# Kernel tuning notes

Hardware: AMD Instinct MI355X
Metric: run time of the kernel (lower is better)

The kernel has to match this reference:

```python
import jax, jax.numpy as jnp
import numpy as np

COST_CLASS, COST_BBOX, COST_MASK = 1.0, 5.0, 2.0
EPS = 1e-6


def setup_inputs() -> dict:
    key = jax.random.key(0)
    k = jax.random.split(key, 8)
    B, Q, M, C1, H, W = 8, 300, 100, 81, 128, 128
    pred_logits = jax.random.normal(k[0], (B, Q, C1), jnp.float32)
    # boxes as valid xyxy in [0,1]: lo in [0,.5], size in [0,.5]
    plo = jax.random.uniform(k[1], (B, Q, 2)) * 0.5
    psz = jax.random.uniform(k[2], (B, Q, 2)) * 0.5
    pred_boxes = jnp.concatenate([plo, plo + psz], axis=-1)
    pred_masks = jax.random.normal(k[3], (B, Q, H, W), jnp.float32)
    gt_labels = jax.random.randint(k[4], (B, M), 0, C1, dtype=jnp.int32)
    glo = jax.random.uniform(k[5], (B, M, 2)) * 0.5
    gsz = jax.random.uniform(k[6], (B, M, 2)) * 0.5
    gt_boxes = jnp.concatenate([glo, glo + gsz], axis=-1)
    gt_masks = (jax.random.uniform(k[7], (B, M, H, W)) > 0.5).astype(jnp.float32)
    valid = jnp.ones((B, M), jnp.bool_)
    return dict(pred_logits=pred_logits, pred_boxes=pred_boxes, pred_masks=pred_masks,
                gt_labels=gt_labels, gt_boxes=gt_boxes, gt_masks=gt_masks, valid=valid)


def _giou(b1, b2):
    # b1 [Q,4], b2 [M,4] (xyxy) -> [Q,M] generalized IoU
    lt = jnp.maximum(b1[:, None, :2], b2[None, :, :2])
    rb = jnp.minimum(b1[:, None, 2:], b2[None, :, 2:])
    wh = jnp.clip(rb - lt, 0.0)
    inter = wh[..., 0] * wh[..., 1]
    a1 = (b1[:, 2] - b1[:, 0]) * (b1[:, 3] - b1[:, 1])
    a2 = (b2[:, 2] - b2[:, 0]) * (b2[:, 3] - b2[:, 1])
    union = a1[:, None] + a2[None, :] - inter
    iou = inter / (union + EPS)
    ltm = jnp.minimum(b1[:, None, :2], b2[None, :, :2])
    rbm = jnp.maximum(b1[:, None, 2:], b2[None, :, 2:])
    whm = jnp.clip(rbm - ltm, 0.0)
    am = whm[..., 0] * whm[..., 1]
    return iou - (am - union) / (am + EPS)


@jax.jit
def _cost_matrix(pred_logits, pred_boxes, pred_masks, gt_labels, gt_boxes, gt_masks):
    B, Q = pred_logits.shape[:2]
    M = gt_labels.shape[1]
    probs = jax.nn.softmax(pred_logits, axis=-1)                      # [B,Q,C+1]
    idx = jnp.broadcast_to(gt_labels[:, None, :].astype(jnp.int32), (B, Q, M))
    cost_class = -jnp.take_along_axis(probs, idx, axis=2)             # [B,Q,M]
    # L1 cdist
    cost_bbox = jnp.abs(pred_boxes[:, :, None, :] - gt_boxes[:, None, :, :]).sum(-1)
    cost_giou = -jax.vmap(_giou)(pred_boxes, gt_boxes)                # [B,Q,M]
    # dice cost
    pm = jax.nn.sigmoid(pred_masks).reshape(B, Q, -1)                 # [B,Q,HW]
    gm = gt_masks.reshape(B, M, -1).astype(pm.dtype)                  # [B,M,HW]
    num = 2.0 * jnp.einsum('bqc,bmc->bqm', pm, gm)
    den = pm.sum(-1)[:, :, None] + gm.sum(-1)[:, None, :]
    cost_mask = 1.0 - num / (den + EPS)
    # NOTE: faithful to source quirk -- giou term is folded into cost_bbox
    # and therefore weighted by COST_BBOX.
    return (COST_CLASS * cost_class + COST_BBOX * (cost_bbox + cost_giou)
            + COST_MASK * cost_mask)


def _hungarian(cost):
    # Jonker-Volgenant style shortest-augmenting-path assignment (e-maxx).
    # cost: np [n,m] with n <= m. Returns p[m]: row assigned to each col (-1 if none).
    n, m = cost.shape
    u = np.zeros(n)
    v = np.zeros(m)
    p = np.full(m, -1, np.int64)
    for i in range(n):
        minv = np.full(m, np.inf)
        way = np.full(m, -1, np.int64)
        used = np.zeros(m, bool)
        cur_row, j0 = i, -1
        while True:
            cur = cost[cur_row] - u[cur_row] - v
            upd = (~used) & (cur < minv)
            minv[upd] = cur[upd]
            way[upd] = j0
            mv = np.where(used, np.inf, minv)
            j1 = int(np.argmin(mv))
            delta = mv[j1]
            u[i] += delta
            uj = np.nonzero(used)[0]
            if uj.size:
                u[p[uj]] += delta
                v[uj] -= delta
            minv[~used] -= delta
            used[j1] = True
            j0 = j1
            cur_row = p[j1]
            if cur_row == -1:
                break
        j = j0
        while j != -1:
            jp = way[j]
            p[j] = p[jp] if jp != -1 else i
            j = jp
    return p


def reference(pred_logits, pred_boxes, pred_masks, gt_labels, gt_boxes, gt_masks, valid):
    # valid is all-ones (num_gt == max_objects for every sample), so the
    # per-sample variable-size slicing in the torch loop reduces to full M.
    C = _cost_matrix(pred_logits, pred_boxes, pred_masks, gt_labels, gt_boxes, gt_masks)
    Cn = np.asarray(C, dtype=np.float64)
    preds, gts = [], []
    for b in range(Cn.shape[0]):
        # solve on transpose: rows = gt (M=100) <= cols = queries (Q=300)
        p = _hungarian(Cn[b].T)            # p[q] = matched gt index or -1
        q = np.nonzero(p >= 0)[0]          # sorted pred indices (scipy convention)
        preds.append(q)
        gts.append(p[q])
    pred_idx = jnp.asarray(np.stack(preds), dtype=jnp.int32)  # [B, M]
    gt_idx = jnp.asarray(np.stack(gts), dtype=jnp.int32)      # [B, M]
    return C, pred_idx, gt_idx
```

## Files before the change

### kernel.cpp

```cpp
#include <hip/hip_runtime.h>

#define HW 16384
#define NQ 300
#define NM 100
#define NB 8
#define NC 81
#define KCH 1024
#define NKC 16
#define CTP 304

typedef __attribute__((ext_vector_type(8))) short frag8;
typedef __attribute__((ext_vector_type(4))) float float4v;
typedef __attribute__((ext_vector_type(4))) unsigned short ushort4v;

__device__ __forceinline__ unsigned short f2bf(float f) {
  union { float f; unsigned u; } c; c.f = f;
  unsigned r = c.u + 0x7FFFu + ((c.u >> 16) & 1u);
  return (unsigned short)(r >> 16);
}

__global__ __launch_bounds__(256) void gmprep_kernel(
    const float* __restrict__ gmask, unsigned short* __restrict__ gm,
    float* __restrict__ gsum) {
  int row = blockIdx.x;
  int t = threadIdx.x;
  const float4v* src = (const float4v*)(gmask + (size_t)row * HW);
  unsigned short* dst = gm + (size_t)row * HW;
  float s = 0.f;
  for (int i = t; i < HW / 4; i += 256) {
    float4v x = src[i];
    s += (x.x + x.y) + (x.z + x.w);
    ushort4v o = { f2bf(x.x), f2bf(x.y), f2bf(x.z), f2bf(x.w) };
    *(ushort4v*)(dst + i * 4) = o;
  }
  for (int off = 32; off > 0; off >>= 1) s += __shfl_xor(s, off, 64);
  __shared__ float red[4];
  int wave = t >> 6, lane = t & 63;
  if (lane == 0) red[wave] = s;
  __syncthreads();
  if (t == 0) gsum[row] = (red[0] + red[1]) + (red[2] + red[3]);
}

__global__ __launch_bounds__(256) void softmax_kernel(
    const float* __restrict__ logits, float* __restrict__ probs) {
  int wave = threadIdx.x >> 6, lane = threadIdx.x & 63;
  int row = blockIdx.x * 4 + wave;
  const float* in = logits + (size_t)row * NC;
  float x0 = (lane < NC) ? in[lane] : -1e30f;
  float x1 = (lane + 64 < NC) ? in[lane + 64] : -1e30f;
  float mx = fmaxf(x0, x1);
  for (int off = 32; off > 0; off >>= 1) mx = fmaxf(mx, __shfl_xor(mx, off, 64));
  float e0 = (lane < NC) ? __expf(x0 - mx) : 0.f;
  float e1 = (lane + 64 < NC) ? __expf(x1 - mx) : 0.f;
  float s = e0 + e1;
  for (int off = 32; off > 0; off >>= 1) s += __shfl_xor(s, off, 64);
  float inv = 1.f / s;
  if (lane < NC) probs[(size_t)row * NC + lane] = e0 * inv;
  if (lane + 64 < NC) probs[(size_t)row * NC + lane + 64] = e1 * inv;
}

__global__ __launch_bounds__(64) void dot_kernel(
    const float* __restrict__ pmask, const unsigned short* __restrict__ gm,
    float* __restrict__ dotv, float* __restrict__ psum) {
  int qt = blockIdx.x;
  int b = blockIdx.y >> 4, kc = blockIdx.y & 15;
  int lane = threadIdx.x;
  int q0 = qt * 16;
  int row_a = q0 + (lane & 15);
  int ra = (row_a < NQ) ? row_a : NQ - 1;
  int koff = (lane >> 4) * 8;
  const float* pA = pmask + ((size_t)b * NQ + ra) * HW + kc * KCH + koff;
  const unsigned short* pB0 = gm + (size_t)b * NM * HW + kc * KCH + koff;
  const unsigned short* pB[7];
#pragma unroll
  for (int mt = 0; mt < 7; ++mt) {
    int row_b = mt * 16 + (lane & 15);
    int rb = (row_b < NM) ? row_b : NM - 1;
    pB[mt] = pB0 + (size_t)rb * HW;
  }
  float4v acc[7];
#pragma unroll
  for (int mt = 0; mt < 7; ++mt) acc[mt] = (float4v){0.f, 0.f, 0.f, 0.f};
  float asum = 0.f;
#pragma unroll 2
  for (int k = 0; k < KCH; k += 32) {
    float4v x0 = *(const float4v*)(pA + k);
    float4v x1 = *(const float4v*)(pA + k + 4);
    float s0 = 1.f / (1.f + __expf(-x0.x));
    float s1 = 1.f / (1.f + __expf(-x0.y));
    float s2 = 1.f / (1.f + __expf(-x0.z));
    float s3 = 1.f / (1.f + __expf(-x0.w));
    float s4 = 1.f / (1.f + __expf(-x1.x));
    float s5 = 1.f / (1.f + __expf(-x1.y));
    float s6 = 1.f / (1.f + __expf(-x1.z));
    float s7 = 1.f / (1.f + __expf(-x1.w));
    asum += ((s0 + s1) + (s2 + s3)) + ((s4 + s5) + (s6 + s7));
    frag8 a;
    a[0] = (short)f2bf(s0); a[1] = (short)f2bf(s1);
    a[2] = (short)f2bf(s2); a[3] = (short)f2bf(s3);
    a[4] = (short)f2bf(s4); a[5] = (short)f2bf(s5);
    a[6] = (short)f2bf(s6); a[7] = (short)f2bf(s7);
#pragma unroll
    for (int mt = 0; mt < 7; ++mt) {
      frag8 bb = *(const frag8*)(pB[mt] + k);
      acc[mt] = __builtin_amdgcn_mfma_f32_16x16x32_bf16(a, bb, acc[mt], 0, 0, 0);
    }
  }
  if (row_a < NQ) unsafeAtomicAdd(&psum[b * NQ + row_a], asum);
#pragma unroll
  for (int mt = 0; mt < 7; ++mt) {
    int cm = mt * 16 + (lane & 15);
    if (cm < NM) {
#pragma unroll
      for (int r = 0; r < 4; ++r) {
        int cq = q0 + (lane >> 4) * 4 + r;
        if (cq < NQ)
          unsafeAtomicAdd(&dotv[((size_t)b * NQ + cq) * NM + cm], acc[mt][r]);
      }
    }
  }
}

__global__ __launch_bounds__(256) void combine_kernel(
    const float* __restrict__ dotv, const float* __restrict__ psum,
    const float* __restrict__ gsum, const float* __restrict__ probs,
    const int* __restrict__ labels, const float* __restrict__ pboxes,
    const float* __restrict__ gboxes, float* __restrict__ outC,
    float* __restrict__ ct) {
  int idx = blockIdx.x * 256 + threadIdx.x;
  if (idx >= NB * NQ * NM) return;
  int b = idx / (NQ * NM);
  int r = idx - b * (NQ * NM);
  int q = r / NM;
  int m = r - q * NM;
  float num = 2.f * dotv[idx];
  float den = psum[b * NQ + q] + gsum[b * NM + m];
  float cmask = 1.f - num / (den + 1e-6f);
  int lab = labels[b * NM + m];
  float cclass = -probs[((size_t)b * NQ + q) * NC + lab];
  const float* pb = pboxes + ((size_t)b * NQ + q) * 4;
  const float* gb = gboxes + ((size_t)b * NM + m) * 4;
  float p0 = pb[0], p1 = pb[1], p2 = pb[2], p3 = pb[3];
  float g0 = gb[0], g1 = gb[1], g2 = gb[2], g3 = gb[3];
  float cbbox = fabsf(p0 - g0) + fabsf(p1 - g1) + fabsf(p2 - g2) + fabsf(p3 - g3);
  float iw = fmaxf(fminf(p2, g2) - fmaxf(p0, g0), 0.f);
  float ih = fmaxf(fminf(p3, g3) - fmaxf(p1, g1), 0.f);
  float inter = iw * ih;
  float a1 = (p2 - p0) * (p3 - p1), a2 = (g2 - g0) * (g3 - g1);
  float uni = a1 + a2 - inter;
  float iou = inter / (uni + 1e-6f);
  float aw = fmaxf(fmaxf(p2, g2) - fminf(p0, g0), 0.f);
  float ah = fmaxf(fmaxf(p3, g3) - fminf(p1, g1), 0.f);
  float am = aw * ah;
  float giou = iou - (am - uni) / (am + 1e-6f);
  float C = cclass + 5.f * (cbbox - giou) + 2.f * cmask;
  outC[idx] = C;
  ct[((size_t)b * NM + m) * CTP + q] = C;
}

__device__ __forceinline__ float wave_fmin_bcast(float x) {
  int t;
  t = __builtin_amdgcn_update_dpp(__float_as_int(x), __float_as_int(x), 0x111, 0xf, 0xf, false);
  x = fminf(x, __int_as_float(t));
  t = __builtin_amdgcn_update_dpp(__float_as_int(x), __float_as_int(x), 0x112, 0xf, 0xf, false);
  x = fminf(x, __int_as_float(t));
  t = __builtin_amdgcn_update_dpp(__float_as_int(x), __float_as_int(x), 0x114, 0xf, 0xf, false);
  x = fminf(x, __int_as_float(t));
  t = __builtin_amdgcn_update_dpp(__float_as_int(x), __float_as_int(x), 0x118, 0xf, 0xf, false);
  x = fminf(x, __int_as_float(t));
  t = __builtin_amdgcn_update_dpp(__float_as_int(x), __float_as_int(x), 0x142, 0xf, 0xf, false);
  x = fminf(x, __int_as_float(t));
  t = __builtin_amdgcn_update_dpp(__float_as_int(x), __float_as_int(x), 0x143, 0xf, 0xf, false);
  x = fminf(x, __int_as_float(t));
  return __int_as_float(__builtin_amdgcn_readlane(__float_as_int(x), 63));
}

extern __shared__ char hsmem[];
__global__ __launch_bounds__(64) void hungarian_kernel(
    const float* __restrict__ ct, float* __restrict__ out) {
  float* cost   = (float*)hsmem;
  float* u      = (float*)(hsmem + 121600);
  int*   p      = (int*)(hsmem + 122000);
  int*   way    = (int*)(hsmem + 123280);
  int*   colOwn = (int*)(hsmem + 124560);
  int*   queue  = (int*)(hsmem + 125840);
  int*   qmisc  = (int*)(hsmem + 127440);
  int*   flist  = colOwn;
  const int b = blockIdx.x;
  const int lane = threadIdx.x;
  const float INF = __builtin_inff();

  {
    const float4v* a4 = (const float4v*)(ct + (size_t)b * NM * CTP);
    float4v* c4 = (float4v*)cost;
    for (int i = lane; i < NM * CTP / 4; i += 64) c4[i] = a4[i];
  }
#pragma unroll
  for (int w = 0; w < 5; ++w) {
    p[lane + 64 * w] = -1;
    colOwn[lane + 64 * w] = 0x7fffffff;
  }
  if (lane == 0) { qmisc[0] = 0; qmisc[1] = 0; }
  float v[5];
#pragma unroll
  for (int w = 0; w < 5; ++w) v[w] = 0.f;
  __syncthreads();

  int rarg0 = 0, rarg1 = 0;
  {
    int i = lane;
    float mv = INF; int cj = 0;
    for (int j = 0; j < NQ; ++j) {
      float c = cost[i * CTP + j];
      if (c < mv) { mv = c; cj = j; }
    }
    u[i] = mv; rarg0 = cj;
  }
  if (lane < NM - 64) {
    int i = lane + 64;
    float mv = INF; int cj = 0;
    for (int j = 0; j < NQ; ++j) {
      float c = cost[i * CTP + j];
      if (c < mv) { mv = c; cj = j; }
    }
    u[i] = mv; rarg1 = cj;
  }
  atomicMin(&colOwn[rarg0], lane);
  if (lane < NM - 64) atomicMin(&colOwn[rarg1], lane + 64);
  __syncthreads();
  int free0 = 0, free1 = 0;
  {
    bool won = (colOwn[rarg0] == lane);
    if (won) p[rarg0] = lane;
    if (lane < NM) {}
    free0 = won ? 0 : 1;
  }
  int rowUsed0 = free0 ? 0 : 1;
  int rowUsed1 = 0;
  if (lane < NM - 64) {
    bool won = (colOwn[rarg1] == lane + 64);
    if (won) p[rarg1] = lane + 64;
    rowUsed1 = won ? 1 : 0;
    free1 = won ? 0 : 1;
  }
  __shared__ int rowUsedA[NM];
  rowUsedA[lane < NM ? lane : 0] = 0;
  rowUsedA[lane] = rowUsed0;
  if (lane < NM - 64) rowUsedA[lane + 64] = rowUsed1;
  {
    unsigned long long m0 = __ballot(free0 != 0);
    if (free0) queue[__popcll(m0 & ((1ull << lane) - 1ull))] = lane;
    int base = (int)__popcll(m0);
    unsigned long long m1 = __ballot(free1 != 0);
    if (free1) queue[base + (int)__popcll(m1 & ((1ull << lane) - 1ull))] = lane + 64;
    base += (int)__popcll(m1);
    if (lane == 0) qmisc[1] = base;
  }

  int pops = 0;
  while (true) {
    __syncthreads();
    int h = qmisc[0], t = qmisc[1];
    if (h >= t || pops >= 192) break;
    int i = queue[h];
    ++pops;
    if (lane == 0) qmisc[0] = h + 1;
    float tv[5];
    float m1 = INF, m2 = INF;
#pragma unroll
    for (int w = 0; w < 5; ++w) {
      int j = lane + 64 * w;
      float tt = (j < NQ) ? (cost[i * CTP + j] - v[w]) : INF;
      tv[w] = tt;
      if (tt < m1) { m2 = m1; m1 = tt; } else if (tt < m2) m2 = tt;
    }
    float m1g = wave_fmin_bcast(m1);
    int j1 = -1;
#pragma unroll
    for (int w = 0; w < 5; ++w) {
      unsigned long long mk = __ballot(tv[w] == m1g);
      if (j1 < 0 && mk) j1 = (int)__builtin_ctzll(mk) + 64 * w;
    }
    float c2c = INF;
#pragma unroll
    for (int w = 0; w < 5; ++w)
      if (lane + 64 * w != j1) c2c = fminf(c2c, tv[w]);
    float c2 = wave_fmin_bcast(c2c);
    float delta = (c2 > m1g) ? (c2 - m1g) : 0.f;
    int i1 = p[j1];
    if (i1 >= 0 && delta <= 0.f) {
      if (lane == 0) u[i] = c2;
      continue;
    }
#pragma unroll
    for (int w = 0; w < 5; ++w) if (lane + 64 * w == j1) v[w] -= delta;
    if (lane == 0) {
      u[i] = c2;
      p[j1] = i;
      rowUsedA[i] = 1;
      if (i1 >= 0) { rowUsedA[i1] = 0; queue[t] = i1; qmisc[1] = t + 1; }
    }
  }
  __syncthreads();

  int nfree;
  {
    int r0 = rowUsedA[lane];
    int r1 = (lane < NM - 64) ? rowUsedA[lane + 64] : 1;
    unsigned long long m0 = __ballot(r0 == 0);
    if (!r0) flist[__popcll(m0 & ((1ull << lane) - 1ull))] = lane;
    int base = (int)__popcll(m0);
    unsigned long long m1 = __ballot(r1 == 0);
    if (!r1) flist[base + (int)__popcll(m1 & ((1ull << lane) - 1ull))] = lane + 64;
    nfree = base + (int)__popcll(m1);
  }
  __syncthreads();

  int pr0, pr1, pr2, pr3, pr4;
  float ur0, ur1;
  pr0 = p[lane]; pr1 = p[lane + 64]; pr2 = p[lane + 128];
  pr3 = p[lane + 192]; pr4 = p[lane + 256];
  ur0 = u[lane];
  ur1 = (lane < NM - 64) ? u[lane + 64] : 0.f;

  for (int fi = 0; fi < nfree; ++fi) {
    int i = flist[fi];
    float dv[5]; int usedR[5];
#pragma unroll
    for (int w = 0; w < 5; ++w) {
      int j = lane + 64 * w;
      dv[w] = INF;
      usedR[w] = (j >= NQ) ? 1 : 0;
      way[j] = -1;
    }
    float S = 0.f;
    int nr = i, j0 = -1;
    while (true) {
      float urow;
      {
        int bits = (nr < 64)
            ? __builtin_amdgcn_readlane(__float_as_int(ur0), nr & 63)
            : __builtin_amdgcn_readlane(__float_as_int(ur1), nr & 63);
        urow = __int_as_float(bits);
      }
      int base = nr * CTP;
      float c0 = cost[base + lane];
      float c1 = cost[base + lane + 64];
      float c2_ = cost[base + lane + 128];
      float c3 = cost[base + lane + 192];
      float c4 = cost[base + lane + 256];
      float cr[5] = {c0, c1, c2_, c3, c4};
      float cmin = INF;
#pragma unroll
      for (int w = 0; w < 5; ++w) {
        if (!usedR[w]) {
          float cand = S + cr[w] - urow - v[w];
          if (cand < dv[w]) { dv[w] = cand; way[lane + 64 * w] = j0; }
          cmin = fminf(cmin, dv[w]);
        }
      }
      float m = wave_fmin_bcast(cmin);
      int j1 = -1;
#pragma unroll
      for (int w = 0; w < 5; ++w) {
        unsigned long long mk = __ballot(!usedR[w] && dv[w] == m);
        if (j1 < 0 && mk) j1 = (int)__builtin_ctzll(mk) + 64 * w;
      }
      S = m;
#pragma unroll
      for (int w = 0; w < 5; ++w) if (lane + 64 * w == j1) usedR[w] = 1;
      j0 = j1;
      int nr2;
      {
        int sl = j1 >> 6, ln = j1 & 63;
        if (sl == 0)      nr2 = __builtin_amdgcn_readlane(pr0, ln);
        else if (sl == 1) nr2 = __builtin_amdgcn_readlane(pr1, ln);
        else if (sl == 2) nr2 = __builtin_amdgcn_readlane(pr2, ln);
        else if (sl == 3) nr2 = __builtin_amdgcn_readlane(pr3, ln);
        else              nr2 = __builtin_amdgcn_readlane(pr4, ln);
      }
      if (nr2 < 0) break;
      nr = nr2;
    }
#pragma unroll
    for (int w = 0; w < 5; ++w) {
      int j = lane + 64 * w;
      if (j < NQ && usedR[w]) {
        float amt = S - dv[w];
        v[w] -= amt;
        int pj = (w == 0) ? pr0 : (w == 1) ? pr1 : (w == 2) ? pr2
               : (w == 3) ? pr3 : pr4;
        if (pj >= 0) u[pj] += amt;
      }
    }
    if (lane == 0) u[i] += S;
    __syncthreads();
    if (lane == 0) {
      int j = j0;
      while (j != -1) {
        int jp = way[j];
        p[j] = (jp != -1) ? p[jp] : i;
        j = jp;
      }
    }
    __syncthreads();
    pr0 = p[lane]; pr1 = p[lane + 64]; pr2 = p[lane + 128];
    pr3 = p[lane + 192]; pr4 = p[lane + 256];
    ur0 = u[lane];
    ur1 = (lane < NM - 64) ? u[lane + 64] : 0.f;
  }

  {
    float* po = out + NB * NQ * NM + b * NM;
    float* go = out + NB * NQ * NM + NB * NM + b * NM;
    int base = 0;
    int prw[5] = {pr0, pr1, pr2, pr3, pr4};
#pragma unroll
    for (int w = 0; w < 5; ++w) {
      int j = lane + 64 * w;
      int pj = (j < NQ) ? prw[w] : -1;
      unsigned long long mask = __ballot(pj >= 0);
      if (pj >= 0) {
        int pos = base + (int)__popcll(mask & ((1ull << lane) - 1ull));
        po[pos] = (float)j;
        go[pos] = (float)pj;
      }
      base += (int)__popcll(mask);
    }
  }
}

extern "C" void kernel_launch(void* const* d_in, const int* in_sizes, int n_in,
                              void* d_out, int out_size, void* d_ws, size_t ws_size,
                              hipStream_t stream) {
  const float* logits = (const float*)d_in[0];
  const float* pboxes = (const float*)d_in[1];
  const float* pmask  = (const float*)d_in[2];
  const int*   labels = (const int*)d_in[3];
  const float* gboxes = (const float*)d_in[4];
  const float* gmask  = (const float*)d_in[5];
  float* out = (float*)d_out;
  char* ws = (char*)d_ws;

  unsigned short* gmb  = (unsigned short*)(ws + 0);
  float* dotv  = (float*)(ws + 26214400);
  float* psum  = (float*)(ws + 27174400);
  float* gsum  = (float*)(ws + 27184000);
  float* probs = (float*)(ws + 27187200);
  float* ct    = (float*)(ws + 27964800);

  hipFuncSetAttribute(reinterpret_cast<const void*>(hungarian_kernel),
                      hipFuncAttributeMaxDynamicSharedMemorySize, 127472);

  hipMemsetAsync(dotv, 0, NB * NQ * NM * sizeof(float) + NB * NQ * sizeof(float), stream);
  hipLaunchKernelGGL(gmprep_kernel, dim3(NB * NM), dim3(256), 0, stream,
                     gmask, gmb, gsum);
  hipLaunchKernelGGL(softmax_kernel, dim3(600), dim3(256), 0, stream, logits, probs);
  hipLaunchKernelGGL(dot_kernel, dim3(19, NB * NKC), dim3(64), 0, stream,
                     pmask, gmb, dotv, psum);
  hipLaunchKernelGGL(combine_kernel, dim3((NB * NQ * NM + 255) / 256), dim3(256), 0, stream,
                     dotv, psum, gsum, probs, labels, pboxes, gboxes, out, ct);
  hipLaunchKernelGGL(hungarian_kernel, dim3(NB), dim3(64), 127472, stream, ct, out);
}
```

Before: 471.1 us.

## Split dot kernel M-tiles across four waves per block and use fast reciprocal

```diff
diff --git a/kernel.cpp b/kernel.cpp
--- a/kernel.cpp
+++ b/kernel.cpp
@@ -59,63 +59,84 @@
   if (lane + 64 < NC) probs[(size_t)row * NC + lane + 64] = e1 * inv;
 }
 
-__global__ __launch_bounds__(64) void dot_kernel(
+__global__ __launch_bounds__(256) void dot_kernel(
     const float* __restrict__ pmask, const unsigned short* __restrict__ gm,
     float* __restrict__ dotv, float* __restrict__ psum) {
   int qt = blockIdx.x;
   int b = blockIdx.y >> 4, kc = blockIdx.y & 15;
-  int lane = threadIdx.x;
+  int tid = threadIdx.x;
+  int wv = tid >> 6, lane = tid & 63;
   int q0 = qt * 16;
   int row_a = q0 + (lane & 15);
   int ra = (row_a < NQ) ? row_a : NQ - 1;
   int koff = (lane >> 4) * 8;
   const float* pA = pmask + ((size_t)b * NQ + ra) * HW + kc * KCH + koff;
   const unsigned short* pB0 = gm + (size_t)b * NM * HW + kc * KCH + koff;
-  const unsigned short* pB[7];
-#pragma unroll
-  for (int mt = 0; mt < 7; ++mt) {
-    int row_b = mt * 16 + (lane & 15);
-    int rb = (row_b < NM) ? row_b : NM - 1;
-    pB[mt] = pB0 + (size_t)rb * HW;
-  }
-  float4v acc[7];
-#pragma unroll
-  for (int mt = 0; mt < 7; ++mt) acc[mt] = (float4v){0.f, 0.f, 0.f, 0.f};
+  int mtbase = 2 * wv;
+  int nmt = (wv < 3) ? 2 : 1;
+  const unsigned short* pBa;
+  const unsigned short* pBb;
+  {
+    int rb0 = mtbase * 16 + (lane & 15);
+    if (rb0 >= NM) rb0 = NM - 1;
+    pBa = pB0 + (size_t)rb0 * HW;
+    int mt1 = mtbase + 1; if (mt1 > 6) mt1 = 6;
+    int rb1 = mt1 * 16 + (lane & 15);
+    if (rb1 >= NM) rb1 = NM - 1;
+    pBb = pB0 + (size_t)rb1 * HW;
+  }
+  float4v acc0 = (float4v){0.f, 0.f, 0.f, 0.f};
+  float4v acc1 = (float4v){0.f, 0.f, 0.f, 0.f};
   float asum = 0.f;
 #pragma unroll 2
   for (int k = 0; k < KCH; k += 32) {
     float4v x0 = *(const float4v*)(pA + k);
     float4v x1 = *(const float4v*)(pA + k + 4);
-    float s0 = 1.f / (1.f + __expf(-x0.x));
-    float s1 = 1.f / (1.f + __expf(-x0.y));
-    float s2 = 1.f / (1.f + __expf(-x0.z));
-    float s3 = 1.f / (1.f + __expf(-x0.w));
-    float s4 = 1.f / (1.f + __expf(-x1.x));
-    float s5 = 1.f / (1.f + __expf(-x1.y));
-    float s6 = 1.f / (1.f + __expf(-x1.z));
-    float s7 = 1.f / (1.f + __expf(-x1.w));
+    float s0 = __builtin_amdgcn_rcpf(1.f + __expf(-x0.x));
+    float s1 = __builtin_amdgcn_rcpf(1.f + __expf(-x0.y));
+    float s2 = __builtin_amdgcn_rcpf(1.f + __expf(-x0.z));
+    float s3 = __builtin_amdgcn_rcpf(1.f + __expf(-x0.w));
+    float s4 = __builtin_amdgcn_rcpf(1.f + __expf(-x1.x));
+    float s5 = __builtin_amdgcn_rcpf(1.f + __expf(-x1.y));
+    float s6 = __builtin_amdgcn_rcpf(1.f + __expf(-x1.z));
+    float s7 = __builtin_amdgcn_rcpf(1.f + __expf(-x1.w));
     asum += ((s0 + s1) + (s2 + s3)) + ((s4 + s5) + (s6 + s7));
     frag8 a;
     a[0] = (short)f2bf(s0); a[1] = (short)f2bf(s1);
     a[2] = (short)f2bf(s2); a[3] = (short)f2bf(s3);
     a[4] = (short)f2bf(s4); a[5] = (short)f2bf(s5);
     a[6] = (short)f2bf(s6); a[7] = (short)f2bf(s7);
-#pragma unroll
-    for (int mt = 0; mt < 7; ++mt) {
-      frag8 bb = *(const frag8*)(pB[mt] + k);
-      acc[mt] = __builtin_amdgcn_mfma_f32_16x16x32_bf16(a, bb, acc[mt], 0, 0, 0);
-    }
-  }
-  if (row_a < NQ) unsafeAtomicAdd(&psum[b * NQ + row_a], asum);
-#pragma unroll
-  for (int mt = 0; mt < 7; ++mt) {
-    int cm = mt * 16 + (lane & 15);
+    frag8 b0 = *(const frag8*)(pBa + k);
+    acc0 = __builtin_amdgcn_mfma_f32_16x16x32_bf16(a, b0, acc0, 0, 0, 0);
+    if (nmt > 1) {
+      frag8 b1 = *(const frag8*)(pBb + k);
+      acc1 = __builtin_amdgcn_mfma_f32_16x16x32_bf16(a, b1, acc1, 0, 0, 0);
+    }
+  }
+  if (wv == 0) {
+    asum += __shfl_xor(asum, 16, 64);
+    asum += __shfl_xor(asum, 32, 64);
+    if (lane < 16 && row_a < NQ) unsafeAtomicAdd(&psum[b * NQ + row_a], asum);
+  }
+  {
+    int cm = mtbase * 16 + (lane & 15);
     if (cm < NM) {
 #pragma unroll
       for (int r = 0; r < 4; ++r) {
         int cq = q0 + (lane >> 4) * 4 + r;
         if (cq < NQ)
-          unsafeAtomicAdd(&dotv[((size_t)b * NQ + cq) * NM + cm], acc[mt][r]);
+          unsafeAtomicAdd(&dotv[((size_t)b * NQ + cq) * NM + cm], acc0[r]);
+      }
+    }
+  }
+  if (nmt > 1) {
+    int cm = (mtbase + 1) * 16 + (lane & 15);
+    if (cm < NM) {
+#pragma unroll
+      for (int r = 0; r < 4; ++r) {
+        int cq = q0 + (lane >> 4) * 4 + r;
+        if (cq < NQ)
+          unsafeAtomicAdd(&dotv[((size_t)b * NQ + cq) * NM + cm], acc1[r]);
       }
     }
   }
@@ -232,7 +253,6 @@
   {
     bool won = (colOwn[rarg0] == lane);
     if (won) p[rarg0] = lane;
-    if (lane < NM) {}
     free0 = won ? 0 : 1;
   }
   int rowUsed0 = free0 ? 0 : 1;
@@ -456,7 +476,7 @@
   hipLaunchKernelGGL(gmprep_kernel, dim3(NB * NM), dim3(256), 0, stream,
                      gmask, gmb, gsum);
   hipLaunchKernelGGL(softmax_kernel, dim3(600), dim3(256), 0, stream, logits, probs);
-  hipLaunchKernelGGL(dot_kernel, dim3(19, NB * NKC), dim3(64), 0, stream,
+  hipLaunchKernelGGL(dot_kernel, dim3(19, NB * NKC), dim3(256), 0, stream,
                      pmask, gmb, dotv, psum);
   hipLaunchKernelGGL(combine_kernel, dim3((NB * NQ * NM + 255) / 256), dim3(256), 0, stream,
                      dotv, psum, gsum, probs, labels, pboxes, gboxes, out, ct);
```

Result: slower. 515.1 us (+9.3%).
